# Kernel optimization log

Measured on AMD Instinct MI355X. Metric: run time of the kernel, lower is better.

The kernel has to match this reference:

```python
import jax, jax.numpy as jnp
import numpy as np

B, S, D, H = 2, 2048, 2048, 16
HD = D // H  # 128
THETA = 10000.0


def _rope_cos_sin(seq_len, head_dim):
    # matches LlamaRotaryEmbedding: inv_freq = 1/theta^(2i/d), emb = cat(freqs, freqs)
    inv_freq = 1.0 / (THETA ** (jnp.arange(0, head_dim, 2, dtype=jnp.float32) / head_dim))
    t = jnp.arange(seq_len, dtype=jnp.float32)
    freqs = jnp.einsum('s,d->sd', t, inv_freq)          # [S, HD/2]
    emb = jnp.concatenate([freqs, freqs], axis=-1)       # [S, HD]
    return jnp.cos(emb), jnp.sin(emb)


def _rotate_half(x):
    x1, x2 = jnp.split(x, 2, axis=-1)
    return jnp.concatenate([-x2, x1], axis=-1)


def setup_inputs() -> dict:
    key = jax.random.key(0)
    ks = jax.random.split(key, 5)
    scale = D ** -0.5
    x = jax.random.normal(ks[0], (B, S, D), jnp.float32)
    wq = jax.random.normal(ks[1], (D, D), jnp.float32) * scale
    wk = jax.random.normal(ks[2], (D, D), jnp.float32) * scale
    wv = jax.random.normal(ks[3], (D, D), jnp.float32) * scale
    wo = jax.random.normal(ks[4], (D, D), jnp.float32) * scale
    # additive causal mask (0 on/below diagonal, large negative above)
    causal = jnp.tril(jnp.ones((S, S), dtype=bool))
    mask = jnp.where(causal, 0.0, -1e9).astype(jnp.float32)[None, None]  # [1,1,S,S]
    return {"x": x, "wq": wq, "wk": wk, "wv": wv, "wo": wo, "mask": mask}


def reference(x, wq, wk, wv, wo, mask):
    b, s, d = x.shape
    # projections + head split: [b, H, s, HD]
    q = (x @ wq).reshape(b, s, H, HD).transpose(0, 2, 1, 3)
    k = (x @ wk).reshape(b, s, H, HD).transpose(0, 2, 1, 3)
    v = (x @ wv).reshape(b, s, H, HD).transpose(0, 2, 1, 3)
    # inline RoPE on q and k (positions 0..s-1 along the seq axis)
    cos, sin = _rope_cos_sin(s, HD)
    cos = cos[None, None]  # [1,1,s,HD]
    sin = sin[None, None]
    q = q * cos + _rotate_half(q) * sin
    k = k * cos + _rotate_half(k) * sin
    # eager attention: QK^T * scale + mask -> softmax -> @ V
    attn = jnp.einsum('bhqd,bhkd->bhqk', q, k) * (HD ** -0.5)
    attn = jax.nn.softmax(attn + mask, axis=-1)
    out = jnp.einsum('bhqk,bhkd->bhqd', attn, v)
    out = out.transpose(0, 2, 1, 3).reshape(b, s, d)
    return out @ wo
```

## Files before the change

kernel.cpp:

```cpp
#include <hip/hip_runtime.h>

#define S_LEN 2048
#define D_DIM 2048
#define NH 16
#define HD 128
#define NB 2
#define NROW (NB * S_LEN)
#define QKV_STR 6144

typedef unsigned short bf16;
typedef __attribute__((ext_vector_type(8))) short bf16x8;
typedef __attribute__((ext_vector_type(4))) float f32x4;
typedef __attribute__((ext_vector_type(16))) float f32x16;
typedef __attribute__((address_space(3))) unsigned int as3u;
typedef __attribute__((address_space(1))) unsigned int as1u;

__device__ __forceinline__ void gload16(const void* g, void* l) {
  __builtin_amdgcn_global_load_lds((const as1u*)g, (as3u*)l, 16, 0, 0);
}

__device__ __forceinline__ unsigned short f2bf(float f) {
  unsigned u = __builtin_bit_cast(unsigned, f);
  u += 0x7FFFu + ((u >> 16) & 1u);
  return (unsigned short)(u >> 16);
}
__device__ __forceinline__ float bf2f(unsigned short b) {
  return __builtin_bit_cast(float, (unsigned)b << 16);
}
__device__ __forceinline__ unsigned cvtpk(float lo, float hi) {
  unsigned r;
  asm("v_cvt_pk_bf16_f32 %0, %1, %2" : "=v"(r) : "v"(lo), "v"(hi));
  return r;
}
__device__ __forceinline__ float exp2a(float x) {
  float r;
  asm("v_exp_f32 %0, %1" : "=v"(r) : "v"(x));
  return r;
}


__global__ void rope_table_k(float2* __restrict__ tab) {
  int i = blockIdx.x * 256 + threadIdx.x;
  int s = i >> 6, d = i & 63;
  float invf = powf(10000.0f, -(float)d * (1.0f / 64.0f));
  float ang = (float)s * invf;
  tab[i] = make_float2(cosf(ang), sinf(ang));
}

__global__ void convert_x_k(const float* __restrict__ src, bf16* __restrict__ dst) {
  int i = (blockIdx.x * 256 + threadIdx.x) * 4;
  float4 v = *(const float4*)(src + i);
  ushort4 w;
  w.x = f2bf(v.x); w.y = f2bf(v.y); w.z = f2bf(v.z); w.w = f2bf(v.w);
  *(ushort4*)(dst + i) = w;
}

__global__ void transpose_w_k(const float* __restrict__ W, bf16* __restrict__ Wt) {
  __shared__ float t[64][65];
  int c0 = blockIdx.x * 64, r0 = blockIdx.y * 64;
  int tx = threadIdx.x & 63, ty = threadIdx.x >> 6;
#pragma unroll
  for (int i = 0; i < 16; ++i)
    t[ty + i * 4][tx] = W[(size_t)(r0 + ty + i * 4) * D_DIM + c0 + tx];
  __syncthreads();
#pragma unroll
  for (int i = 0; i < 16; ++i)
    Wt[(size_t)(c0 + ty + i * 4) * D_DIM + r0 + tx] = f2bf(t[tx][ty + i * 4]);
}

__global__ void transpose_v_k(const bf16* __restrict__ Vsrc, bf16* __restrict__ Vt) {
  __shared__ bf16 t[64][65];
  int bh = blockIdx.z;
  int b = bh >> 4, h = bh & 15;
  int s0 = blockIdx.x * 64, d0 = blockIdx.y * 64;
  int tx = threadIdx.x & 63, ty = threadIdx.x >> 6;
  const bf16* src = Vsrc + (size_t)(b * S_LEN + s0) * QKV_STR + h * HD + d0;
#pragma unroll
  for (int i = 0; i < 16; ++i)
    t[ty + i * 4][tx] = src[(size_t)(ty + i * 4) * QKV_STR + tx];
  __syncthreads();
  bf16* dst = Vt + ((size_t)bh * HD + d0) * S_LEN + s0;
#pragma unroll
  for (int i = 0; i < 16; ++i)
    dst[(size_t)(ty + i * 4) * S_LEN + tx] = t[tx][ty + i * 4];
}

__global__ void rope_apply_k(bf16* __restrict__ qkv, const float2* __restrict__ tab) {
  int i = blockIdx.x * 256 + threadIdx.x;
  int d = i & 63;
  int t = i >> 6;
  int h = t & 15;
  int row = t >> 4;
  int s = row & (S_LEN - 1);
  const float qscale = 0.12751743f;
  float2 cs = tab[s * 64 + d];
  size_t base = (size_t)row * QKV_STR + h * HD + d;
  float x1 = bf2f(qkv[base]), x2 = bf2f(qkv[base + 64]);
  qkv[base]      = f2bf((x1 * cs.x - x2 * cs.y) * qscale);
  qkv[base + 64] = f2bf((x2 * cs.x + x1 * cs.y) * qscale);
  size_t kb2 = base + 2048;
  float y1 = bf2f(qkv[kb2]), y2 = bf2f(qkv[kb2 + 64]);
  qkv[kb2]      = f2bf(y1 * cs.x - y2 * cs.y);
  qkv[kb2 + 64] = f2bf(y2 * cs.x + y1 * cs.y);
}


__device__ __forceinline__ void storec(bf16* p, float v) { *p = f2bf(v); }
__device__ __forceinline__ void storec(float* p, float v) { *p = v; }

template <typename OutT>
__global__ __launch_bounds__(256) void gemm_bt_k(
    const bf16* __restrict__ A, const bf16* __restrict__ Bt,
    OutT* __restrict__ C, int M, int N, int K) {
  __shared__ bf16 As[128 * 32];
  __shared__ bf16 Bs[128 * 32];
  const int tid = threadIdx.x;
  const int lane = tid & 63;
  const int wid = tid >> 6;
  const int bm = blockIdx.y * 128;
  const int bn = blockIdx.x * 128;
  const int wr = (wid >> 1) * 64;
  const int wc = (wid & 1) * 64;
  const int lr = lane & 15;
  const int kg = lane >> 4;

  f32x4 acc[4][4] = {};

  const int c0 = wid * 2;
  const int srow = lane >> 2;
  const int scol = (lane & 3) * 8;
  const bf16* Ap0 = A + (size_t)(bm + c0 * 16 + srow) * K + scol;
  const bf16* Ap1 = Ap0 + (size_t)16 * K;
  const bf16* Bp0 = Bt + (size_t)(bn + c0 * 16 + srow) * K + scol;
  const bf16* Bp1 = Bp0 + (size_t)16 * K;
  bf16* Asd0 = &As[c0 * 512];
  bf16* Asd1 = &As[(c0 + 1) * 512];
  bf16* Bsd0 = &Bs[c0 * 512];
  bf16* Bsd1 = &Bs[(c0 + 1) * 512];

  for (int k0 = 0; k0 < K; k0 += 32) {
    __syncthreads();
    gload16(Ap0 + k0, Asd0);
    gload16(Ap1 + k0, Asd1);
    gload16(Bp0 + k0, Bsd0);
    gload16(Bp1 + k0, Bsd1);
    __syncthreads();
    bf16x8 a[4], b[4];
#pragma unroll
    for (int m = 0; m < 4; ++m)
      a[m] = *(const bf16x8*)&As[(wr + m * 16 + lr) * 32 + kg * 8];
#pragma unroll
    for (int n = 0; n < 4; ++n)
      b[n] = *(const bf16x8*)&Bs[(wc + n * 16 + lr) * 32 + kg * 8];
#pragma unroll
    for (int m = 0; m < 4; ++m)
#pragma unroll
      for (int n = 0; n < 4; ++n)
        acc[m][n] = __builtin_amdgcn_mfma_f32_16x16x32_bf16(a[m], b[n], acc[m][n], 0, 0, 0);
  }

#pragma unroll
  for (int m = 0; m < 4; ++m) {
    int row0 = bm + wr + m * 16 + kg * 4;
#pragma unroll
    for (int n = 0; n < 4; ++n) {
      int col = bn + wc + n * 16 + lr;
#pragma unroll
      for (int r = 0; r < 4; ++r)
        storec(&C[(size_t)(row0 + r) * N + col], acc[m][n][r]);
    }
  }
}

#define FBODY(T, CUR0, CUR1, NXT0, NXT1)                                         \
  {                                                                              \
    const int kv0_ = (T) * 64;                                                   \
    stageV(kv0_ + 64, ((T) + 1) & 1);                                            \
    stageK(kv0_ + 128, (T) & 1);                                                 \
    if (kv0_ + 64 <= qw0 + 31) {                                                 \
      NXT0 = 0.0f; NXT1 = 0.0f;                                                  \
      const bf16* krow0_ = &sh[(((T) + 1) & 1) * 8192] + (size_t)l31 * 128;      \
      const bf16* krow1_ = krow0_ + 32 * 128;                                    \
      _Pragma("unroll")                                                          \
      for (int ks = 0; ks < 8; ++ks) {                                           \
        int cb_ = ((ks * 32) ^ kxor) >> 1;                                       \
        bf16x8 kf0_ = *(const bf16x8*)(krow0_ + cb_);                            \
        bf16x8 kf1_ = *(const bf16x8*)(krow1_ + cb_);                            \
        NXT0 = __builtin_amdgcn_mfma_f32_32x32x16_bf16(kf0_, qf[ks], NXT0, 0, 0, 0); \
        NXT1 = __builtin_amdgcn_mfma_f32_32x32x16_bf16(kf1_, qf[ks], NXT1, 0, 0, 0); \
      }                                                                          \
    }                                                                            \
    if (kv0_ <= qw0 + 31) {                                                      \
      if (kv0_ + 63 > qw0) {                                                     \
        _Pragma("unroll")                                                        \
        for (int r = 0; r < 16; ++r) {                                           \
          int kvg_ = kv0_ + (r & 3) + 8 * (r >> 2) + 4 * h;                      \
          if (kvg_ > q) CUR0[r] = -3.0e38f;                                      \
          if (kvg_ + 32 > q) CUR1[r] = -3.0e38f;                                 \
        }                                                                        \
      }                                                                          \
      float tm_[8];                                                              \
      _Pragma("unroll")                                                          \
      for (int r = 0; r < 8; ++r)                                                \
        tm_[r] = fmaxf(fmaxf(CUR0[r], CUR0[r + 8]), fmaxf(CUR1[r], CUR1[r + 8])); \
      _Pragma("unroll")                                                          \
      for (int r = 0; r < 4; ++r) tm_[r] = fmaxf(tm_[r], tm_[r + 4]);            \
      float mt_ = fmaxf(fmaxf(tm_[0], tm_[1]), fmaxf(tm_[2], tm_[3]));           \
      mt_ = fmaxf(mt_, __shfl_xor(mt_, 32));                                     \
      if (__any(mt_ > m_run + 8.0f)) {                                           \
        float mnew_ = fmaxf(m_run, mt_);                                         \
        float alpha_ = exp2a(m_run - mnew_);                                     \
        l_run *= alpha_;                                                         \
        _Pragma("unroll")                                                        \
        for (int n = 0; n < 4; ++n)                                              \
          _Pragma("unroll")                                                      \
          for (int r = 0; r < 16; ++r) ot[n][r] *= alpha_;                       \
        m_run = mnew_;                                                           \
      }                                                                          \
      float rs_[16];                                                             \
      _Pragma("unroll")                                                          \
      for (int r = 0; r < 16; ++r) {                                             \
        CUR0[r] = exp2a(CUR0[r] - m_run);                                        \
        CUR1[r] = exp2a(CUR1[r] - m_run);                                        \
        rs_[r] = CUR0[r] + CUR1[r];                                              \
      }                                                                          \
      _Pragma("unroll")                                                          \
      for (int r = 0; r < 8; ++r) rs_[r] += rs_[r + 8];                          \
      _Pragma("unroll")                                                          \
      for (int r = 0; r < 4; ++r) rs_[r] += rs_[r + 4];                          \
      float rsum_ = (rs_[0] + rs_[1]) + (rs_[2] + rs_[3]);                       \
      rsum_ += __shfl_xor(rsum_, 32);                                            \
      l_run += rsum_;                                                            \
      unsigned wd0_[8], wd1_[8];                                                 \
      _Pragma("unroll")                                                          \
      for (int j = 0; j < 8; ++j) {                                              \
        wd0_[j] = cvtpk(CUR0[2 * j], CUR0[2 * j + 1]);                           \
        wd1_[j] = cvtpk(CUR1[2 * j], CUR1[2 * j + 1]);                           \
      }                                                                          \
      const bf16* Vbuf_ = &sh[16384 + ((T) & 1) * 8192];                         \
      _Pragma("unroll")                                                          \
      for (int t4 = 0; t4 < 4; ++t4) {                                           \
        const unsigned* wdp_ = (t4 >> 1) ? wd1_ : wd0_;                          \
        int a0_ = 4 * (t4 & 1) + 2 * h;                                          \
        int sidx_ = 4 * (t4 & 1) + 2 * (1 - h);                                  \
        unsigned s0_ = (unsigned)__shfl_xor((int)wdp_[sidx_], 32);               \
        unsigned s1_ = (unsigned)__shfl_xor((int)wdp_[sidx_ + 1], 32);           \
        unsigned pb4_[4];                                                        \
        pb4_[0] = h ? s0_ : wdp_[a0_];                                           \
        pb4_[1] = h ? s1_ : wdp_[a0_ + 1];                                       \
        pb4_[2] = h ? wdp_[a0_] : s0_;                                           \
        pb4_[3] = h ? wdp_[a0_ + 1] : s1_;                                       \
        bf16x8 pb_ = __builtin_bit_cast(bf16x8, *(uint4*)pb4_);                  \
        int cb_ = ((t4 * 32) ^ vxor) >> 1;                                       \
        _Pragma("unroll")                                                        \
        for (int n = 0; n < 4; ++n) {                                            \
          bf16x8 va_ = *(const bf16x8*)(Vbuf_ + (size_t)(32 * n + l31) * 64 + cb_); \
          ot[n] = __builtin_amdgcn_mfma_f32_32x32x16_bf16(va_, pb_, ot[n], 0, 0, 0); \
        }                                                                        \
      }                                                                          \
    }                                                                            \
    asm volatile("s_waitcnt vmcnt(0)" ::: "memory");                             \
    __builtin_amdgcn_s_barrier();                                                \
    __builtin_amdgcn_sched_barrier(0);                                           \
  }

__global__ __launch_bounds__(256, 2) void flash_attn_k(
    const bf16* __restrict__ Q, const bf16* __restrict__ Kb,
    const bf16* __restrict__ Vt, bf16* __restrict__ O) {
  __shared__ bf16 sh[32768];
  const int tid = threadIdx.x;
  const int lane = tid & 63;
  const int w = tid >> 6;
  const int h = lane >> 5;
  const int l31 = lane & 31;
  const int bh = blockIdx.y;
  const int b = bh >> 4;
  const int hh = bh & 15;
  const int qb = (gridDim.x - 1 - blockIdx.x) * 128;
  const int qw0 = qb + 32 * w;
  const int q = qw0 + l31;

  const bf16* qp = Q + (size_t)(b * S_LEN + q) * QKV_STR + hh * HD + h * 8;
  bf16x8 qf[8];
#pragma unroll
  for (int ks = 0; ks < 8; ++ks) qf[ks] = *(const bf16x8*)(qp + ks * 16);

  f32x16 ot[4] = {};
  float m_run = -3.0e38f, l_run = 0.f;

  const bf16* Kg = Kb + (size_t)(b * S_LEN) * QKV_STR + hh * HD;
  const bf16* Vg = Vt + (size_t)bh * HD * S_LEN;

  const int kst_row = 16 * w + (lane >> 4);
  const int vst_row = 32 * w + (lane >> 3);
  const int vst_col = (((lane & 7) ^ (lane >> 3)) << 3);
  const int kxor = (16 * h) ^ ((l31 & 15) << 4);
  const int vxor = (16 * h) ^ ((l31 & 7) << 4);

  auto stageK = [&](int kv0, int buf) {
#pragma unroll
    for (int jj = 0; jj < 4; ++jj) {
      int kr = (kv0 + kst_row + jj * 4) & (S_LEN - 1);
      gload16(Kg + (size_t)kr * QKV_STR + (((lane & 15) ^ (jj * 4 + (lane >> 4))) << 3),
              &sh[buf * 8192 + (16 * w + jj * 4) * 128]);
    }
  };
  auto stageV = [&](int kv0, int buf) {
    int c = (kv0 & (S_LEN - 1)) + vst_col;
#pragma unroll
    for (int jj = 0; jj < 4; ++jj) {
      int vr = vst_row + jj * 8;
      gload16(Vg + (size_t)vr * S_LEN + c, &sh[16384 + buf * 8192 + (32 * w + jj * 8) * 64]);
    }
  };

  stageK(0, 0);
  stageV(0, 0);
  stageK(64, 1);
  asm volatile("s_waitcnt vmcnt(8)" ::: "memory");
  __builtin_amdgcn_s_barrier();
  __builtin_amdgcn_sched_barrier(0);

  f32x16 stA0 = 0.0f, stA1 = 0.0f, stB0, stB1;
  {
    const bf16* krow0 = &sh[0] + (size_t)l31 * 128;
    const bf16* krow1 = krow0 + 32 * 128;
#pragma unroll
    for (int ks = 0; ks < 8; ++ks) {
      int cb = ((ks * 32) ^ kxor) >> 1;
      bf16x8 kf0 = *(const bf16x8*)(krow0 + cb);
      bf16x8 kf1 = *(const bf16x8*)(krow1 + cb);
      stA0 = __builtin_amdgcn_mfma_f32_32x32x16_bf16(kf0, qf[ks], stA0, 0, 0, 0);
      stA1 = __builtin_amdgcn_mfma_f32_32x32x16_bf16(kf1, qf[ks], stA1, 0, 0, 0);
    }
  }
  asm volatile("s_waitcnt vmcnt(0)" ::: "memory");
  __builtin_amdgcn_s_barrier();
  __builtin_amdgcn_sched_barrier(0);

  const int nt = qb / 64 + 2;
  int t = 0;
  for (; t + 1 < nt; t += 2) {
    FBODY(t, stA0, stA1, stB0, stB1);
    FBODY(t + 1, stB0, stB1, stA0, stA1);
  }
  if (t < nt) FBODY(t, stA0, stA1, stB0, stB1);

  float inv = 1.0f / l_run;
  bf16* ow = &sh[w * 4096];
#pragma unroll
  for (int n = 0; n < 4; ++n)
#pragma unroll
    for (int rq = 0; rq < 4; ++rq) {
      int dbase = 32 * n + 8 * rq + 4 * h;
      unsigned u0 = cvtpk(ot[n][4 * rq + 0] * inv, ot[n][4 * rq + 1] * inv);
      unsigned u1 = cvtpk(ot[n][4 * rq + 2] * inv, ot[n][4 * rq + 3] * inv);
      uint2 uu = make_uint2(u0, u1);
      *(uint2*)(ow + l31 * 128 + (dbase ^ ((l31 & 15) << 3))) = uu;
    }
  __syncthreads();
#pragma unroll
  for (int p = 0; p < 8; ++p) {
    int qr = p * 4 + (lane >> 4);
    int ce = ((((lane & 15) << 4) ^ ((qr & 15) << 4)) >> 1);
    bf16x8 vrow = *(const bf16x8*)(ow + qr * 128 + ce);
    *(bf16x8*)(O + (size_t)(b * S_LEN + qw0 + qr) * D_DIM + hh * HD + (lane & 15) * 8) = vrow;
  }
}


extern "C" void kernel_launch(void* const* d_in, const int* in_sizes, int n_in,
                              void* d_out, int out_size, void* d_ws, size_t ws_size,
                              hipStream_t stream) {
  (void)in_sizes; (void)n_in; (void)out_size; (void)ws_size;
  const float* x  = (const float*)d_in[0];
  const float* wq = (const float*)d_in[1];
  const float* wk = (const float*)d_in[2];
  const float* wv = (const float*)d_in[3];
  const float* wo = (const float*)d_in[4];
  float* out = (float*)d_out;

  char* ws = (char*)d_ws;
  const size_t MB = 1u << 20;
  bf16* xb    = (bf16*)(ws + 0 * MB);
  bf16* Ob    = xb;
  bf16* wTall = (bf16*)(ws + 16 * MB);
  bf16* wTo   = (bf16*)(ws + 40 * MB);
  bf16* QKV   = (bf16*)(ws + 48 * MB);
  bf16* Vtb   = (bf16*)(ws + 96 * MB);
  float2* tab = (float2*)(ws + 112 * MB);

  rope_table_k<<<512, 256, 0, stream>>>(tab);
  convert_x_k<<<8192, 256, 0, stream>>>(x, xb);
  dim3 tg(32, 32);
  transpose_w_k<<<tg, 256, 0, stream>>>(wq, wTall);
  transpose_w_k<<<tg, 256, 0, stream>>>(wk, wTall + (size_t)2048 * D_DIM);
  transpose_w_k<<<tg, 256, 0, stream>>>(wv, wTall + (size_t)4096 * D_DIM);
  transpose_w_k<<<tg, 256, 0, stream>>>(wo, wTo);

  gemm_bt_k<bf16><<<dim3(QKV_STR / 128, NROW / 128), 256, 0, stream>>>(
      xb, wTall, QKV, NROW, QKV_STR, D_DIM);

  rope_apply_k<<<16384, 256, 0, stream>>>(QKV, tab);
  transpose_v_k<<<dim3(32, 2, 32), 256, 0, stream>>>(QKV + 4096, Vtb);

  flash_attn_k<<<dim3(S_LEN / 128, NB * NH), 256, 0, stream>>>(
      QKV, QKV + 2048, Vtb, Ob);

  gemm_bt_k<float><<<dim3(D_DIM / 128, NROW / 128), 256, 0, stream>>>(
      Ob, wTo, out, NROW, D_DIM, D_DIM);
}
```

Baseline: 349.9 us.

## Replace QKV projection GEMM with 256x256-tile pipelined 8-wave kernel

Adds a new GEMM kernel for the fused QKV projection. It uses 256x256 output tiles, 512 threads and double-buffered LDS staging through global_load_lds. Each k-step is split into four MFMA phases that interleave LDS fragment reads with async prefetch of the next tiles, using explicit barriers, waitcnt and setprio scheduling. The goal is more operand reuse per tile and better overlap of memory traffic with MFMA work. The cost is 128KB of LDS per block and fragile hand-tuned synchronisation that could race if the wait counts are wrong.

```diff
diff --git a/kernel.cpp b/kernel.cpp
--- a/kernel.cpp
+++ b/kernel.cpp
@@ -168,6 +168,117 @@
 #pragma unroll
       for (int r = 0; r < 4; ++r)
         storec(&C[(size_t)(row0 + r) * N + col], acc[m][n][r]);
+    }
+  }
+}
+
+
+#define PH_READ_A(DST, FB, P)                                                  \
+  _Pragma("unroll") for (int mm = 0; mm < 4; ++mm)                             \
+    _Pragma("unroll") for (int ks = 0; ks < 2; ++ks)                           \
+      DST[mm][ks] = *(const bf16x8*)&smem[(P)*16384 + wm * 8192 +              \
+                                          (((FB) + mm) * 2 + ks) * 512 + lane * 8];
+#define PH_READ_B(DST, NFB, P)                                                 \
+  _Pragma("unroll") for (int j = 0; j < 2; ++j)                                \
+    _Pragma("unroll") for (int ks = 0; ks < 2; ++ks)                           \
+      DST[j][ks] = *(const bf16x8*)&smem[32768 + (P)*16384 + hb * 8192 +       \
+                                         ((wn1 * 4 + (NFB) + j) * 2 + ks) * 512 + lane * 8];
+#define STAGE_A(KT, H, P)                                                      \
+  { int k0_ = ((KT) & 31) * 64;                                                \
+    gload16(Apt + (H)*262144 + k0_, &smem[(P)*16384 + (H)*8192 + w * 512]);    \
+    gload16(Apt + (H)*262144 + 131072 + k0_,                                   \
+            &smem[(P)*16384 + (H)*8192 + (8 + w) * 512]); }
+#define STAGE_B(KT, H, P)                                                      \
+  { int k0_ = ((KT) & 31) * 64;                                                \
+    gload16(Bpt + (H)*262144 + k0_, &smem[32768 + (P)*16384 + (H)*8192 + w * 512]); \
+    gload16(Bpt + (H)*262144 + 131072 + k0_,                                   \
+            &smem[32768 + (P)*16384 + (H)*8192 + (8 + w) * 512]); }
+#define MFMA_Q(AF, BF, MB, NB)                                                 \
+  _Pragma("unroll") for (int mm = 0; mm < 4; ++mm)                             \
+    _Pragma("unroll") for (int j = 0; j < 2; ++j)                              \
+      _Pragma("unroll") for (int ks = 0; ks < 2; ++ks)                         \
+        acc[(MB) + mm][(NB) + j] = __builtin_amdgcn_mfma_f32_16x16x32_bf16(    \
+            AF[mm][ks], BF[j][ks], acc[(MB) + mm][(NB) + j], 0, 0, 0);
+#define PH_TAIL                                                                \
+  __builtin_amdgcn_s_barrier();                                                \
+  asm volatile("s_waitcnt lgkmcnt(0)" ::: "memory");                           \
+  __builtin_amdgcn_sched_barrier(0);                                           \
+  __builtin_amdgcn_s_setprio(1);
+#define PH_END                                                                 \
+  __builtin_amdgcn_s_setprio(0);                                               \
+  __builtin_amdgcn_s_barrier();
+
+#define GROUP(KT, P)                                                           \
+  {                                                                            \
+    bf16x8 a0[4][2], a1[4][2], b0[2][2], b1[2][2];                             \
+                                                       \
+    PH_READ_A(a0, 0, P); PH_READ_B(b0, 0, P);                                  \
+    STAGE_B((KT) + 1, 1, (P) ^ 1);                                             \
+    PH_TAIL                                                                    \
+    MFMA_Q(a0, b0, 0, 0);                                                      \
+    PH_END                                                                     \
+                                                       \
+    PH_READ_A(a1, 4, P);                                                       \
+    PH_TAIL                                                                    \
+    MFMA_Q(a1, b0, 4, 0);                                                      \
+    PH_END                                                                     \
+                                                       \
+    PH_READ_B(b1, 2, P);                                                       \
+    STAGE_A((KT) + 2, 0, P); STAGE_A((KT) + 2, 1, P);                          \
+    PH_TAIL                                                                    \
+    MFMA_Q(a1, b1, 4, 2);                                                      \
+    PH_END                                                                     \
+                                                       \
+    STAGE_B((KT) + 2, 0, P);                                                   \
+    PH_TAIL                                                                    \
+    MFMA_Q(a0, b1, 0, 2);                                                      \
+    __builtin_amdgcn_s_setprio(0);                                             \
+    asm volatile("s_waitcnt vmcnt(6)" ::: "memory");                           \
+    __builtin_amdgcn_sched_barrier(0);                                         \
+    __builtin_amdgcn_s_barrier();                                              \
+  }
+
+__global__ __launch_bounds__(512, 2) void gemm256_k(
+    const bf16* __restrict__ A, const bf16* __restrict__ Bt,
+    bf16* __restrict__ C, int N) {
+  __shared__ bf16 smem[65536];
+  const int tid = threadIdx.x;
+  const int lane = tid & 63;
+  const int w = tid >> 6;
+  const int wm = w >> 2;
+  const int wn = w & 3;
+  const int wn1 = wn & 1;
+  const int hb = wn >> 1;
+  const int bm = blockIdx.y * 256;
+  const int bn = blockIdx.x * 256;
+
+  const bf16* Apt = A + (size_t)(bm + (w >> 1) * 16 + (lane & 15)) * 2048 +
+                    (w & 1) * 32 + (lane >> 4) * 8;
+  const bf16* Bpt = Bt + (size_t)(bn + (w >> 1) * 16 + (lane & 15)) * 2048 +
+                    (w & 1) * 32 + (lane >> 4) * 8;
+
+  f32x4 acc[8][4] = {};
+
+  STAGE_A(0, 0, 0); STAGE_A(0, 1, 0); STAGE_B(0, 0, 0); STAGE_B(0, 1, 0);
+  STAGE_A(1, 0, 1); STAGE_A(1, 1, 1); STAGE_B(1, 0, 1);
+  asm volatile("s_waitcnt vmcnt(6)" ::: "memory");
+  __builtin_amdgcn_sched_barrier(0);
+  __builtin_amdgcn_s_barrier();
+
+  for (int t = 0; t < 32; t += 2) {
+    GROUP(t, 0);
+    GROUP(t + 1, 1);
+  }
+
+#pragma unroll
+  for (int mF = 0; mF < 8; ++mF) {
+    int row0 = bm + wm * 128 + mF * 16 + (lane >> 4) * 4;
+#pragma unroll
+    for (int nf = 0; nf < 4; ++nf) {
+      int col = bn + wn * 64 + nf * 16 + (lane & 15);
+#pragma unroll
+      for (int r = 0; r < 4; ++r)
+        C[(size_t)(row0 + r) * N + col] = f2bf(acc[mF][nf][r]);
     }
   }
 }
@@ -398,8 +509,8 @@
   transpose_w_k<<<tg, 256, 0, stream>>>(wv, wTall + (size_t)4096 * D_DIM);
   transpose_w_k<<<tg, 256, 0, stream>>>(wo, wTo);
 
-  gemm_bt_k<bf16><<<dim3(QKV_STR / 128, NROW / 128), 256, 0, stream>>>(
-      xb, wTall, QKV, NROW, QKV_STR, D_DIM);
+  gemm256_k<<<dim3(QKV_STR / 256, NROW / 256), 512, 0, stream>>>(
+      xb, wTall, QKV, QKV_STR);
 
   rope_apply_k<<<16384, 256, 0, stream>>>(QKV, tab);
   transpose_v_k<<<dim3(32, 2, 32), 256, 0, stream>>>(QKV + 4096, Vtb);
```

New measurement: 353.9 us. No clear change (+1.2%).
